# Optimization experiments

Hardware: AMD Instinct MI355X
Metric: run time of the kernel (lower is better)

Reference implementation:

```python
import jax, jax.numpy as jnp
import numpy as np

L, E, H, V = 12, 1024, 4096, 50277
LN_EPS = 9.999999747378752e-06  # tf float32 1e-5


def _layernorm(x, w, b):
    m = jnp.mean(x)
    xc = x - m
    return xc / jnp.sqrt(jnp.mean(xc * xc) + LN_EPS) * w + b


def setup_inputs() -> dict:
    key = jax.random.key(0)
    ks = jax.random.split(key, 32)
    f32 = jnp.float32

    def n(i, shape, s=0.02):
        return (jax.random.normal(ks[i], shape, f32) * s).astype(f32)

    inp = {
        "statea": n(0, (L, E), 0.3),
        "stateb": jax.random.uniform(ks[1], (L, E), f32),
        "statec": jax.random.uniform(ks[2], (L, E), f32),
        "stated": n(3, (L, E), 0.3),
        "preprocess": n(4, (V, E), 0.5),
        "ln1w": 1.0 + n(5, (L, E), 0.05),
        "ln1b": n(6, (L, E), 0.05),
        "ln2w": 1.0 + n(7, (L, E), 0.05),
        "ln2b": n(8, (L, E), 0.05),
        "att_key": n(9, (L, E, E)),
        "att_receptance": n(10, (L, E, E)),
        "att_value": n(11, (L, E, E)),
        "kktk": jax.random.uniform(ks[12], (L, E), f32),
        "vvtv": jax.random.uniform(ks[13], (L, E), f32),
        "rrtr": jax.random.uniform(ks[14], (L, E), f32),
        "time_first": n(15, (L, E), 0.2),
        "time_decay": n(16, (L, E), 0.2) - 1.0,
        "outputvv": n(17, (L, E, E)),
        "time_mix_k_ffn": jax.random.uniform(ks[18], (L, E), f32),
        "time_mix_r_ffn": jax.random.uniform(ks[19], (L, E), f32),
        "key_ffn": n(20, (L, H, E)),
        "receptance_ffn": n(21, (L, E, E)),
        "value_ffn": n(22, (L, E, H)),
        "post0": 1.0 + n(23, (E,), 0.05),
        "post1": n(24, (E,), 0.05),
        "post2": n(25, (V, E)),
        "token": 123,
    }
    return inp


def _forward(statea, stateb, statec, stated, preprocess, ln1w, ln1b, ln2w, ln2b,
             att_key, att_receptance, att_value, kktk, vvtv, rrtr, time_first,
             time_decay, outputvv, time_mix_k_ffn, time_mix_r_ffn, key_ffn,
             receptance_ffn, value_ffn, post0, post1, post2, token):
    x0 = preprocess[token]  # [E]

    def step(x, p):
        (sa, sb, sc, sd, l1w, l1b, l2w, l2b, ak, ar, av, kk, vv, rr,
         tfirst, tdecay, ovv, tmk_m, tmr_m, kf, rf, vf) = p
        xy = _layernorm(x, l1w, l1b)
        # WKV time-mixing (single step): mat-vecs + exp-decay state recursion
        k = jnp.exp(ak @ (xy + kk * sa))        # [E]
        v = av @ (xy + vv * sa)                 # [E]
        r = jnp.exp(ar @ (xy + rr * sa)) + 1.0  # [E]
        etf = jnp.exp(tfirst)
        w = sb + etf * k * v
        d = sc * r + etf * k * r
        mvv = ovv @ (w / (d + 0.001))           # [E]
        sxx = x + mvv
        aaa = xy
        etd = jnp.exp(tdecay)
        bbb = sb * etd + k * v
        ccc = sc * etd + k
        # channel-mixing FFN
        xx = _layernorm(sxx, l2w, l2b)
        kma = kf @ (xx + tmk_m * sd)            # [H]
        km = jnp.square(jnp.maximum(kma, 0.0))
        rt = jnp.exp(rf @ (xx + tmr_m * sd)) + 1.0  # [E]
        x_new = sxx + (vf @ km) / rt
        ddd = xx
        return x_new, (aaa, bbb, ccc, ddd)

    xs = (statea, stateb, statec, stated, ln1w, ln1b, ln2w, ln2b, att_key,
          att_receptance, att_value, kktk, vvtv, rrtr, time_first, time_decay,
          outputvv, time_mix_k_ffn, time_mix_r_ffn, key_ffn, receptance_ffn,
          value_ffn)
    xL, (aaa, bbb, ccc, ddd) = jax.lax.scan(step, x0, xs)
    logits = post2 @ _layernorm(xL, post0, post1)  # [V]
    return logits, aaa, bbb, ccc, ddd


def reference(statea, stateb, statec, stated, preprocess, ln1w, ln1b, ln2w, ln2b,
              att_key, att_receptance, att_value, kktk, vvtv, rrtr, time_first,
              time_decay, outputvv, time_mix_k_ffn, time_mix_r_ffn, key_ffn,
              receptance_ffn, value_ffn, post0, post1, post2, token):
    return _forward(statea, stateb, statec, stated, preprocess, ln1w, ln1b,
                    ln2w, ln2b, att_key, att_receptance, att_value, kktk, vvtv,
                    rrtr, time_first, time_decay, outputvv, time_mix_k_ffn,
                    time_mix_r_ffn, key_ffn, receptance_ffn, value_ffn, post0,
                    post1, post2, token)
```

## Files before the change

### kernel.cpp

```cpp
#include <hip/hip_runtime.h>
#include <math.h>


typedef unsigned long long u64;

constexpr int E = 1024;
constexpr int H = 4096;
constexpr int V = 50277;
constexpr int L = 12;
constexpr int NBLK = 256;
constexpr int NTHR = 512;
constexpr float LN_EPS = 9.999999747378752e-06f;

#define SCOPE_AGENT __HIP_MEMORY_SCOPE_AGENT

__device__ __forceinline__ u64 aload(const u64 *p) {
  return __hip_atomic_load(p, __ATOMIC_RELAXED, SCOPE_AGENT);
}
__device__ __forceinline__ void astore(u64 *p, u64 v) {
  __hip_atomic_store(p, v, __ATOMIC_RELAXED, SCOPE_AGENT);
}
__device__ __forceinline__ u64 mkw(unsigned ep, float f) {
  return ((u64)ep << 32) | (u64)__float_as_uint(f);
}
__device__ __forceinline__ float wpay(u64 v) { return __uint_as_float((unsigned)v); }
__device__ __forceinline__ bool freshw(u64 v, unsigned ep) {
  return (unsigned)(v >> 32) == ep;
}

__device__ __forceinline__ void lds_sync() {
  asm volatile("s_waitcnt lgkmcnt(0)" ::: "memory");
  __builtin_amdgcn_s_barrier();
}

struct Args {
  const float *statea, *stateb, *statec, *stated, *pre;
  const float *ln1w, *ln1b, *ln2w, *ln2b;
  const float *ak, *ar, *av, *kk, *vv, *rr, *tf, *td, *ovv;
  const float *tmk, *tmr, *kf, *rf, *vf;
  const float *post0, *post1, *post2;
  const int *token;
  float *out;
  u64 *wu, *wsx, *ssx, *wkm, *wx, *sxs;
};

__device__ __forceinline__ float wred(float v) {
#pragma unroll
  for (int off = 32; off; off >>= 1) v += __shfl_down(v, off, 64);
  return v;
}

__device__ __forceinline__ float dot4(float4 w, float4 x) {
  return w.x * x.x + w.y * x.y + w.z * x.z + w.w * x.w;
}

__device__ __forceinline__ float2 gather2(const u64 *wd, unsigned ep, int tid) {
  const u64 *p = wd + 2 * tid;
  u64 a0 = aload(p), a1 = aload(p + 1);
  while (!(freshw(a0, ep) & freshw(a1, ep))) {
    __builtin_amdgcn_s_sleep(1);
    a0 = aload(p); a1 = aload(p + 1);
  }
  return make_float2(wpay(a0), wpay(a1));
}

__device__ __forceinline__ void gather2s(const u64 *wd, const u64 *st, unsigned ep,
                                         int tid, float2 &v, float &sp) {
  const u64 *p = wd + 2 * tid;
  const u64 *q = st + tid;
  u64 a0 = aload(p), a1 = aload(p + 1), a2 = aload(q);
  while (!(freshw(a0, ep) & freshw(a1, ep) & freshw(a2, ep))) {
    __builtin_amdgcn_s_sleep(1);
    a0 = aload(p); a1 = aload(p + 1); a2 = aload(q);
  }
  v = make_float2(wpay(a0), wpay(a1));
  sp = wpay(a2);
}

__device__ __forceinline__ void gather8(const u64 *wd, unsigned ep, int tid,
                                        float4 &f0, float4 &f1) {
  const u64 *p = wd + 8 * tid;
  u64 b0, b1, b2, b3, b4, b5, b6, b7;
  for (;;) {
    b0 = aload(p);     b1 = aload(p + 1); b2 = aload(p + 2); b3 = aload(p + 3);
    b4 = aload(p + 4); b5 = aload(p + 5); b6 = aload(p + 6); b7 = aload(p + 7);
    bool ok = freshw(b0, ep) & freshw(b1, ep) & freshw(b2, ep) & freshw(b3, ep) &
              freshw(b4, ep) & freshw(b5, ep) & freshw(b6, ep) & freshw(b7, ep);
    if (ok) break;
    __builtin_amdgcn_s_sleep(1);
  }
  f0 = make_float4(wpay(b0), wpay(b1), wpay(b2), wpay(b3));
  f1 = make_float4(wpay(b4), wpay(b5), wpay(b6), wpay(b7));
}

__device__ __forceinline__ float2 stats_from_partials(float sp, float *s_red,
                                                      int lane, int wid) {
#pragma unroll
  for (int m = 2; m <= 32; m <<= 1) sp += __shfl_xor(sp, m, 64);
  if (lane < 2) s_red[wid * 2 + lane] = sp;
  lds_sync();
  float ts = 0.f, ts2 = 0.f;
#pragma unroll
  for (int i = 0; i < 8; ++i) { ts += s_red[2 * i]; ts2 += s_red[2 * i + 1]; }
  float m = ts * (1.0f / E);
  float var = ts2 * (1.0f / E) - m * m;
  return make_float2(m, rsqrtf(var + LN_EPS));
}

__device__ __forceinline__ float2 stats_full(float2 v, float *s_red, int lane, int wid) {
  float s = v.x + v.y, s2 = v.x * v.x + v.y * v.y;
#pragma unroll
  for (int m = 1; m <= 32; m <<= 1) {
    s += __shfl_xor(s, m, 64);
    s2 += __shfl_xor(s2, m, 64);
  }
  if (lane == 0) { s_red[wid * 2] = s; s_red[wid * 2 + 1] = s2; }
  lds_sync();
  float ts = 0.f, ts2 = 0.f;
#pragma unroll
  for (int i = 0; i < 8; ++i) { ts += s_red[2 * i]; ts2 += s_red[2 * i + 1]; }
  float m = ts * (1.0f / E);
  float var = ts2 * (1.0f / E) - m * m;
  return make_float2(m, rsqrtf(var + LN_EPS));
}

struct P1B {
  float4 w[6];
  float2 lw, lb, sa, kk, vv, rr;
  float tf, td, sb, sc;
};

__device__ __forceinline__ void load_p1(P1B &p, const Args &a, int l, int grow,
                                        int b0h, int tid, int blk) {
  const size_t lE = (size_t)l * E;
  const float4 *kr = reinterpret_cast<const float4 *>(a.ak + (lE + grow) * E);
  const float4 *vr = reinterpret_cast<const float4 *>(a.av + (lE + grow) * E);
  const float4 *rr4 = reinterpret_cast<const float4 *>(a.ar + (lE + grow) * E);
  p.w[0] = kr[b0h]; p.w[1] = kr[b0h + 64];
  p.w[2] = vr[b0h]; p.w[3] = vr[b0h + 64];
  p.w[4] = rr4[b0h]; p.w[5] = rr4[b0h + 64];
  p.lw = reinterpret_cast<const float2 *>(a.ln1w + lE)[tid];
  p.lb = reinterpret_cast<const float2 *>(a.ln1b + lE)[tid];
  p.sa = reinterpret_cast<const float2 *>(a.statea + lE)[tid];
  p.kk = reinterpret_cast<const float2 *>(a.kk + lE)[tid];
  p.vv = reinterpret_cast<const float2 *>(a.vv + lE)[tid];
  p.rr = reinterpret_cast<const float2 *>(a.rr + lE)[tid];
  if (tid < 4) {
    size_t o = lE + blk * 4 + tid;
    p.tf = a.tf[o]; p.td = a.td[o]; p.sb = a.stateb[o]; p.sc = a.statec[o];
  } else {
    p.tf = 0.f; p.td = 0.f; p.sb = 0.f; p.sc = 1.f;
  }
}

__device__ __forceinline__ void loadrow(float4 *d, const float4 *P, int r, int lane) {
  const float4 *p = P + (size_t)r * 256;
  d[0] = p[lane]; d[1] = p[lane + 64]; d[2] = p[lane + 128]; d[3] = p[lane + 192];
}

__global__ __launch_bounds__(NTHR, 2) void rwkv_fused(Args a) {
  __shared__ __align__(16) float s_a[4096];
  __shared__ __align__(16) float s_x[1024];
  __shared__ float s_red[16];
  __shared__ float s_pp[24];
  __shared__ float s_rt[4];

  const int tid = threadIdx.x;
  const int lane = tid & 63;
  const int wid = tid >> 6;
  const int blk = blockIdx.x;
  const int rloc = wid >> 1;
  const int h = wid & 1;
  const int grow = blk * 4 + rloc;
  const int b0h = h * 128 + lane;
  const int bv = h * 512 + lane;

  float *out_logits = a.out;
  float *out_aaa = a.out + V;
  float *out_bbb = out_aaa + L * E;
  float *out_ccc = out_bbb + L * E;
  float *out_ddd = out_ccc + L * E;

  const int tok = a.token[0];
  const float *pre_row = a.pre + (size_t)tok * E;
  const float4 *s4a = reinterpret_cast<const float4 *>(s_a);

  P1B p1;
  load_p1(p1, a, 0, grow, b0h, tid, blk);

#pragma unroll 1
  for (int l = 0; l < L; ++l) {
    const size_t lE = (size_t)l * E;
    const unsigned e1 = 4 * l + 1, e2 = 4 * l + 2, e3 = 4 * l + 3, e4 = 4 * l + 4;
    float4 pwo[2], pw3[10], pw4[8];
    float2 e3w, e3b, e3sd, e3tk, e3tr;

    {
      float2 xv; float2 st;
      if (l == 0) {
        xv = reinterpret_cast<const float2 *>(pre_row)[tid];
        reinterpret_cast<float2 *>(s_x)[tid] = xv;
        st = stats_full(xv, s_red, lane, wid);
      } else {
        float sp;
        gather2s(a.wx, a.sxs, 4 * l, tid, xv, sp);
        reinterpret_cast<float2 *>(s_x)[tid] = xv;
        st = stats_from_partials(sp, s_red, lane, wid);
      }
      float2 xy = make_float2((xv.x - st.x) * st.y * p1.lw.x + p1.lb.x,
                              (xv.y - st.x) * st.y * p1.lw.y + p1.lb.y);
      if ((tid >> 1) == blk) {
        out_aaa[lE + 2 * tid] = xy.x;
        out_aaa[lE + 2 * tid + 1] = xy.y;
      }
      reinterpret_cast<float2 *>(s_a)[tid] =
          make_float2(xy.x + p1.kk.x * p1.sa.x, xy.y + p1.kk.y * p1.sa.y);
      reinterpret_cast<float2 *>(s_a + 1024)[tid] =
          make_float2(xy.x + p1.vv.x * p1.sa.x, xy.y + p1.vv.y * p1.sa.y);
      reinterpret_cast<float2 *>(s_a + 2048)[tid] =
          make_float2(xy.x + p1.rr.x * p1.sa.x, xy.y + p1.rr.y * p1.sa.y);
      lds_sync();
      float accK = dot4(p1.w[0], s4a[b0h]) + dot4(p1.w[1], s4a[b0h + 64]);
      float accV = dot4(p1.w[2], s4a[256 + b0h]) + dot4(p1.w[3], s4a[256 + b0h + 64]);
      float accR = dot4(p1.w[4], s4a[512 + b0h]) + dot4(p1.w[5], s4a[512 + b0h + 64]);
      accK = wred(accK); accV = wred(accV); accR = wred(accR);
      if (lane == 0) {
        s_pp[wid * 3 + 0] = accK;
        s_pp[wid * 3 + 1] = accV;
        s_pp[wid * 3 + 2] = accR;
      }
      lds_sync();
      {
        const float4 *orow = reinterpret_cast<const float4 *>(a.ovv + (lE + grow) * E);
        pwo[0] = orow[b0h]; pwo[1] = orow[b0h + 64];
      }
      if (wid == 0) {
        int i = lane & 3;
        float K = s_pp[(2 * i) * 3] + s_pp[(2 * i + 1) * 3];
        float Vv = s_pp[(2 * i) * 3 + 1] + s_pp[(2 * i + 1) * 3 + 1];
        float R = s_pp[(2 * i) * 3 + 2] + s_pp[(2 * i + 1) * 3 + 2];
        float kx = expf(K), rx = expf(R) + 1.0f;
        float etf = expf(p1.tf), etd = expf(p1.td);
        float w_ = p1.sb + etf * kx * Vv;
        float d_ = p1.sc * rx + etf * kx * rx;
        float uv = w_ / (d_ + 0.001f);
        if (lane < 4) {
          size_t o = lE + blk * 4 + lane;
          astore(a.wu + blk * 4 + lane, mkw(e1, uv));
          out_bbb[o] = p1.sb * etd + kx * Vv;
          out_ccc[o] = p1.sc * etd + kx;
        }
      }
    }

    {
      float2 u2 = gather2(a.wu, e1, tid);
      reinterpret_cast<float2 *>(s_a)[tid] = u2;
      lds_sync();
      float acc = dot4(pwo[0], s4a[b0h]) + dot4(pwo[1], s4a[b0h + 64]);
      float x4 = s_x[blk * 4 + (lane & 3)];
      acc = wred(acc);
      if (lane == 0) s_pp[wid] = acc;
      lds_sync();
      {
        const float *kfb = a.kf + (size_t)l * H * E;
        const float4 *k0 = reinterpret_cast<const float4 *>(kfb + (size_t)(blk * 16 + wid) * E);
        const float4 *k1 = reinterpret_cast<const float4 *>(kfb + (size_t)(blk * 16 + 8 + wid) * E);
        pw3[0] = k0[lane];       pw3[1] = k0[lane + 64];
        pw3[2] = k0[lane + 128]; pw3[3] = k0[lane + 192];
        pw3[4] = k1[lane];       pw3[5] = k1[lane + 64];
        pw3[6] = k1[lane + 128]; pw3[7] = k1[lane + 192];
        const float4 *rrow = reinterpret_cast<const float4 *>(a.rf + (lE + grow) * E);
        pw3[8] = rrow[b0h]; pw3[9] = rrow[b0h + 64];
        e3w = reinterpret_cast<const float2 *>(a.ln2w + lE)[tid];
        e3b = reinterpret_cast<const float2 *>(a.ln2b + lE)[tid];
        e3sd = reinterpret_cast<const float2 *>(a.stated + lE)[tid];
        e3tk = reinterpret_cast<const float2 *>(a.tmk + lE)[tid];
        e3tr = reinterpret_cast<const float2 *>(a.tmr + lE)[tid];
      }
      if (wid == 0) {
        int i = lane & 3;
        float sxxv = x4 + s_pp[2 * i] + s_pp[2 * i + 1];
        float s0 = __shfl(sxxv, 0), s1 = __shfl(sxxv, 1);
        float s2v = __shfl(sxxv, 2), s3 = __shfl(sxxv, 3);
        float sum = s0 + s1 + s2v + s3;
        float ssq = s0 * s0 + s1 * s1 + s2v * s2v + s3 * s3;
        if (lane < 4) astore(a.wsx + blk * 4 + lane, mkw(e2, sxxv));
        if (lane == 0) astore(a.ssx + blk * 2 + 0, mkw(e2, sum));
        if (lane == 1) astore(a.ssx + blk * 2 + 1, mkw(e2, ssq));
      }
    }

    {
      float2 sxv; float sp;
      gather2s(a.wsx, a.ssx, e2, tid, sxv, sp);
      reinterpret_cast<float2 *>(s_x)[tid] = sxv;
      float2 st = stats_from_partials(sp, s_red, lane, wid);
      float2 xx = make_float2((sxv.x - st.x) * st.y * e3w.x + e3b.x,
                              (sxv.y - st.x) * st.y * e3w.y + e3b.y);
      if ((tid >> 1) == blk) {
        out_ddd[lE + 2 * tid] = xx.x;
        out_ddd[lE + 2 * tid + 1] = xx.y;
      }
      reinterpret_cast<float2 *>(s_a)[tid] =
          make_float2(xx.x + e3tk.x * e3sd.x, xx.y + e3tk.y * e3sd.y);
      reinterpret_cast<float2 *>(s_a + 1024)[tid] =
          make_float2(xx.x + e3tr.x * e3sd.x, xx.y + e3tr.y * e3sd.y);
      lds_sync();
      float k0 = 0.f, k1 = 0.f;
#pragma unroll
      for (int it = 0; it < 4; ++it) {
        float4 xv4 = s4a[it * 64 + lane];
        k0 += dot4(pw3[it], xv4);
        k1 += dot4(pw3[4 + it], xv4);
      }
      float ar_ = dot4(pw3[8], s4a[256 + b0h]) + dot4(pw3[9], s4a[256 + b0h + 64]);
      k0 = wred(k0); k1 = wred(k1); ar_ = wred(ar_);
      if (lane == 0) {
        float t0 = fmaxf(k0, 0.f), t1 = fmaxf(k1, 0.f);
        astore(a.wkm + blk * 16 + wid, mkw(e3, t0 * t0));
        astore(a.wkm + blk * 16 + 8 + wid, mkw(e3, t1 * t1));
        s_pp[wid] = ar_;
      }
      lds_sync();
      {
        const float4 *vrow = reinterpret_cast<const float4 *>(a.vf + (lE + grow) * H);
        pw4[0] = vrow[bv];       pw4[1] = vrow[bv + 64];
        pw4[2] = vrow[bv + 128]; pw4[3] = vrow[bv + 192];
        pw4[4] = vrow[bv + 256]; pw4[5] = vrow[bv + 320];
        pw4[6] = vrow[bv + 384]; pw4[7] = vrow[bv + 448];
      }
      if (tid < 4) s_rt[tid] = expf(s_pp[2 * tid] + s_pp[2 * tid + 1]) + 1.0f;
    }

    {
      float4 f0, f1;
      gather8(a.wkm, e3, tid, f0, f1);
      reinterpret_cast<float4 *>(s_a)[2 * tid] = f0;
      reinterpret_cast<float4 *>(s_a)[2 * tid + 1] = f1;
      lds_sync();
      float acc = 0.f;
#pragma unroll
      for (int it = 0; it < 8; ++it) acc += dot4(pw4[it], s4a[bv + it * 64]);
      float sx4 = s_x[blk * 4 + (lane & 3)];
      acc = wred(acc);
      if (lane == 0) s_pp[wid] = acc;
      lds_sync();
      if (l + 1 < L) {
        load_p1(p1, a, l + 1, grow, b0h, tid, blk);
      } else {
        p1.lw = reinterpret_cast<const float2 *>(a.post0)[tid];
        p1.lb = reinterpret_cast<const float2 *>(a.post1)[tid];
      }
      if (wid == 0) {
        int i = lane & 3;
        float xn = sx4 + (s_pp[2 * i] + s_pp[2 * i + 1]) / s_rt[i];
        float s0 = __shfl(xn, 0), s1 = __shfl(xn, 1);
        float s2v = __shfl(xn, 2), s3 = __shfl(xn, 3);
        float sum = s0 + s1 + s2v + s3;
        float ssq = s0 * s0 + s1 * s1 + s2v * s2v + s3 * s3;
        if (lane < 4) astore(a.wx + blk * 4 + lane, mkw(e4, xn));
        if (lane == 0) astore(a.sxs + blk * 2 + 0, mkw(e4, sum));
        if (lane == 1) astore(a.sxs + blk * 2 + 1, mkw(e4, ssq));
      }
    }
  }

  {
    float2 xv; float sp;
    gather2s(a.wx, a.sxs, 4 * L, tid, xv, sp);
    float2 st = stats_from_partials(sp, s_red, lane, wid);
    reinterpret_cast<float2 *>(s_a)[tid] =
        make_float2((xv.x - st.x) * st.y * p1.lw.x + p1.lb.x,
                    (xv.y - st.x) * st.y * p1.lw.y + p1.lb.y);
    lds_sync();

    const float4 *P2 = reinterpret_cast<const float4 *>(a.post2);
    const int gw = blk * 8 + wid;
    int r0 = gw, r1 = gw + 2048;
    float4 A0[4], A1[4];
    loadrow(A0, P2, r0, lane);
    loadrow(A1, P2, r1 < V ? r1 : r0, lane);
    while (true) {
      int n0 = r0 + 4096, n1 = n0 + 2048;
      bool more = n0 < V;
      float4 B0[4], B1[4];
      if (more) {
        loadrow(B0, P2, n0, lane);
        loadrow(B1, P2, n1 < V ? n1 : n0, lane);
      }
      float a0 = dot4(A0[0], s4a[lane]) + dot4(A0[1], s4a[lane + 64]) +
                 dot4(A0[2], s4a[lane + 128]) + dot4(A0[3], s4a[lane + 192]);
      float a1 = dot4(A1[0], s4a[lane]) + dot4(A1[1], s4a[lane + 64]) +
                 dot4(A1[2], s4a[lane + 128]) + dot4(A1[3], s4a[lane + 192]);
      a0 = wred(a0); a1 = wred(a1);
      if (lane == 0) {
        out_logits[r0] = a0;
        if (r1 < V) out_logits[r1] = a1;
      }
      if (!more) break;
#pragma unroll
      for (int q = 0; q < 4; ++q) { A0[q] = B0[q]; A1[q] = B1[q]; }
      r0 = n0; r1 = n1;
    }
  }
}

extern "C" void kernel_launch(void *const *d_in, const int *in_sizes, int n_in,
                              void *d_out, int out_size, void *d_ws, size_t ws_size,
                              hipStream_t stream) {
  (void)in_sizes; (void)n_in; (void)out_size; (void)ws_size;
  Args a;
  a.statea = (const float *)d_in[0];
  a.stateb = (const float *)d_in[1];
  a.statec = (const float *)d_in[2];
  a.stated = (const float *)d_in[3];
  a.pre    = (const float *)d_in[4];
  a.ln1w   = (const float *)d_in[5];
  a.ln1b   = (const float *)d_in[6];
  a.ln2w   = (const float *)d_in[7];
  a.ln2b   = (const float *)d_in[8];
  a.ak     = (const float *)d_in[9];
  a.ar     = (const float *)d_in[10];
  a.av     = (const float *)d_in[11];
  a.kk     = (const float *)d_in[12];
  a.vv     = (const float *)d_in[13];
  a.rr     = (const float *)d_in[14];
  a.tf     = (const float *)d_in[15];
  a.td     = (const float *)d_in[16];
  a.ovv    = (const float *)d_in[17];
  a.tmk    = (const float *)d_in[18];
  a.tmr    = (const float *)d_in[19];
  a.kf     = (const float *)d_in[20];
  a.rf     = (const float *)d_in[21];
  a.vf     = (const float *)d_in[22];
  a.post0  = (const float *)d_in[23];
  a.post1  = (const float *)d_in[24];
  a.post2  = (const float *)d_in[25];
  a.token  = (const int *)d_in[26];
  a.out    = (float *)d_out;

  u64 *wb = (u64 *)d_ws;
  a.wu  = wb;
  a.wsx = wb + 1024;
  a.ssx = wb + 2048;
  a.wkm = wb + 2560;
  a.wx  = wb + 6656;
  a.sxs = wb + 7680;
  hipMemsetAsync(d_ws, 0, 8192 * sizeof(u64), stream);
  rwkv_fused<<<NBLK, NTHR, 0, stream>>>(a);
}
```

Baseline: 302.3 us.

## Replace epoch-tagged data words with per-block flag barrier and plain payloads

Replaces the per-element epoch-tagged 64-bit words that consumers spin on with plain float payloads and one padded per-block epoch flag. Wave 0 drains its stores, publishes the flag and polls all 256 block flags, while the other waves prefetch the next stage's weights. Cross-block LayerNorm partial sums are dropped and every block recomputes full stats from the gathered vector. This cuts polled traffic and halves payload size, but turns fine-grained dataflow into a full grid barrier per stage and relies on relaxed-atomic ordering plus vmcnt drains for correctness.

```diff
diff --git a/kernel.cpp b/kernel.cpp
--- a/kernel.cpp
+++ b/kernel.cpp
@@ -3,6 +3,7 @@
 
 
 typedef unsigned long long u64;
+typedef unsigned u32;
 
 constexpr int E = 1024;
 constexpr int H = 4096;
@@ -12,25 +13,29 @@
 constexpr int NTHR = 512;
 constexpr float LN_EPS = 9.999999747378752e-06f;
 
-#define SCOPE_AGENT __HIP_MEMORY_SCOPE_AGENT
-
-__device__ __forceinline__ u64 aload(const u64 *p) {
-  return __hip_atomic_load(p, __ATOMIC_RELAXED, SCOPE_AGENT);
-}
-__device__ __forceinline__ void astore(u64 *p, u64 v) {
-  __hip_atomic_store(p, v, __ATOMIC_RELAXED, SCOPE_AGENT);
-}
-__device__ __forceinline__ u64 mkw(unsigned ep, float f) {
-  return ((u64)ep << 32) | (u64)__float_as_uint(f);
-}
-__device__ __forceinline__ float wpay(u64 v) { return __uint_as_float((unsigned)v); }
-__device__ __forceinline__ bool freshw(u64 v, unsigned ep) {
-  return (unsigned)(v >> 32) == ep;
+#define SA __HIP_MEMORY_SCOPE_AGENT
+
+__device__ __forceinline__ void stf(float *p, float v) {
+  __hip_atomic_store(p, v, __ATOMIC_RELAXED, SA);
+}
+__device__ __forceinline__ void stu(u32 *p, u32 v) {
+  __hip_atomic_store(p, v, __ATOMIC_RELAXED, SA);
+}
+__device__ __forceinline__ u32 ldu(const u32 *p) {
+  return __hip_atomic_load(p, __ATOMIC_RELAXED, SA);
+}
+__device__ __forceinline__ float2 ld2(const float *p) {
+  union { u64 u; float2 f; } c;
+  c.u = __hip_atomic_load((const u64 *)p, __ATOMIC_RELAXED, SA);
+  return c.f;
 }
 
 __device__ __forceinline__ void lds_sync() {
   asm volatile("s_waitcnt lgkmcnt(0)" ::: "memory");
   __builtin_amdgcn_s_barrier();
+}
+__device__ __forceinline__ void vdrain() {
+  asm volatile("s_waitcnt vmcnt(0)" ::: "memory");
 }
 
 struct Args {
@@ -41,7 +46,8 @@
   const float *post0, *post1, *post2;
   const int *token;
   float *out;
-  u64 *wu, *wsx, *ssx, *wkm, *wx, *sxs;
+  u32 *flags;
+  float *wu, *wsx, *wx, *wkm;
 };
 
 __device__ __forceinline__ float wred(float v) {
@@ -49,79 +55,8 @@
   for (int off = 32; off; off >>= 1) v += __shfl_down(v, off, 64);
   return v;
 }
-
 __device__ __forceinline__ float dot4(float4 w, float4 x) {
   return w.x * x.x + w.y * x.y + w.z * x.z + w.w * x.w;
-}
-
-__device__ __forceinline__ float2 gather2(const u64 *wd, unsigned ep, int tid) {
-  const u64 *p = wd + 2 * tid;
-  u64 a0 = aload(p), a1 = aload(p + 1);
-  while (!(freshw(a0, ep) & freshw(a1, ep))) {
-    __builtin_amdgcn_s_sleep(1);
-    a0 = aload(p); a1 = aload(p + 1);
-  }
-  return make_float2(wpay(a0), wpay(a1));
-}
-
-__device__ __forceinline__ void gather2s(const u64 *wd, const u64 *st, unsigned ep,
-                                         int tid, float2 &v, float &sp) {
-  const u64 *p = wd + 2 * tid;
-  const u64 *q = st + tid;
-  u64 a0 = aload(p), a1 = aload(p + 1), a2 = aload(q);
-  while (!(freshw(a0, ep) & freshw(a1, ep) & freshw(a2, ep))) {
-    __builtin_amdgcn_s_sleep(1);
-    a0 = aload(p); a1 = aload(p + 1); a2 = aload(q);
-  }
-  v = make_float2(wpay(a0), wpay(a1));
-  sp = wpay(a2);
-}
-
-__device__ __forceinline__ void gather8(const u64 *wd, unsigned ep, int tid,
-                                        float4 &f0, float4 &f1) {
-  const u64 *p = wd + 8 * tid;
-  u64 b0, b1, b2, b3, b4, b5, b6, b7;
-  for (;;) {
-    b0 = aload(p);     b1 = aload(p + 1); b2 = aload(p + 2); b3 = aload(p + 3);
-    b4 = aload(p + 4); b5 = aload(p + 5); b6 = aload(p + 6); b7 = aload(p + 7);
-    bool ok = freshw(b0, ep) & freshw(b1, ep) & freshw(b2, ep) & freshw(b3, ep) &
-              freshw(b4, ep) & freshw(b5, ep) & freshw(b6, ep) & freshw(b7, ep);
-    if (ok) break;
-    __builtin_amdgcn_s_sleep(1);
-  }
-  f0 = make_float4(wpay(b0), wpay(b1), wpay(b2), wpay(b3));
-  f1 = make_float4(wpay(b4), wpay(b5), wpay(b6), wpay(b7));
-}
-
-__device__ __forceinline__ float2 stats_from_partials(float sp, float *s_red,
-                                                      int lane, int wid) {
-#pragma unroll
-  for (int m = 2; m <= 32; m <<= 1) sp += __shfl_xor(sp, m, 64);
-  if (lane < 2) s_red[wid * 2 + lane] = sp;
-  lds_sync();
-  float ts = 0.f, ts2 = 0.f;
-#pragma unroll
-  for (int i = 0; i < 8; ++i) { ts += s_red[2 * i]; ts2 += s_red[2 * i + 1]; }
-  float m = ts * (1.0f / E);
-  float var = ts2 * (1.0f / E) - m * m;
-  return make_float2(m, rsqrtf(var + LN_EPS));
-}
-
-__device__ __forceinline__ float2 stats_full(float2 v, float *s_red, int lane, int wid) {
-  float s = v.x + v.y, s2 = v.x * v.x + v.y * v.y;
-#pragma unroll
-  for (int m = 1; m <= 32; m <<= 1) {
-    s += __shfl_xor(s, m, 64);
-    s2 += __shfl_xor(s2, m, 64);
-  }
-  if (lane == 0) { s_red[wid * 2] = s; s_red[wid * 2 + 1] = s2; }
-  lds_sync();
-  float ts = 0.f, ts2 = 0.f;
-#pragma unroll
-  for (int i = 0; i < 8; ++i) { ts += s_red[2 * i]; ts2 += s_red[2 * i + 1]; }
-  float m = ts * (1.0f / E);
-  float var = ts2 * (1.0f / E) - m * m;
-  return make_float2(m, rsqrtf(var + LN_EPS));
 }
 
 struct P1B {
@@ -129,7 +64,6 @@
   float2 lw, lb, sa, kk, vv, rr;
   float tf, td, sb, sc;
 };
-
 __device__ __forceinline__ void load_p1(P1B &p, const Args &a, int l, int grow,
                                         int b0h, int tid, int blk) {
   const size_t lE = (size_t)l * E;
@@ -152,6 +86,55 @@
     p.tf = 0.f; p.td = 0.f; p.sb = 0.f; p.sc = 1.f;
   }
 }
+__device__ __forceinline__ void load_ovv_kf0(float4 po[2], float4 pf[8],
+                                             const Args &a, int l, int grow,
+                                             int b0h, int blk, int wid, int lane) {
+  const size_t lE = (size_t)l * E;
+  const float4 *orow = reinterpret_cast<const float4 *>(a.ovv + (lE + grow) * E);
+  po[0] = orow[b0h]; po[1] = orow[b0h + 64];
+  const float *kfb = a.kf + (size_t)l * H * E;
+  const float4 *k0 = reinterpret_cast<const float4 *>(kfb + (size_t)(blk * 16 + wid) * E);
+  pf[0] = k0[lane]; pf[1] = k0[lane + 64]; pf[2] = k0[lane + 128]; pf[3] = k0[lane + 192];
+}
+struct P3B {
+  float4 r[2];
+  float2 lw, lb, sd, tk, tr;
+};
+__device__ __forceinline__ void load_kf1_rf(float4 pf[8], P3B &p, const Args &a,
+                                            int l, int grow, int b0h, int blk,
+                                            int wid, int lane, int tid) {
+  const size_t lE = (size_t)l * E;
+  const float *kfb = a.kf + (size_t)l * H * E;
+  const float4 *k1 = reinterpret_cast<const float4 *>(kfb + (size_t)(blk * 16 + 8 + wid) * E);
+  pf[4] = k1[lane]; pf[5] = k1[lane + 64]; pf[6] = k1[lane + 128]; pf[7] = k1[lane + 192];
+  const float4 *rrow = reinterpret_cast<const float4 *>(a.rf + (lE + grow) * E);
+  p.r[0] = rrow[b0h]; p.r[1] = rrow[b0h + 64];
+  p.lw = reinterpret_cast<const float2 *>(a.ln2w + lE)[tid];
+  p.lb = reinterpret_cast<const float2 *>(a.ln2b + lE)[tid];
+  p.sd = reinterpret_cast<const float2 *>(a.stated + lE)[tid];
+  p.tk = reinterpret_cast<const float2 *>(a.tmk + lE)[tid];
+  p.tr = reinterpret_cast<const float2 *>(a.tmr + lE)[tid];
+}
+__device__ __forceinline__ void load_vf(float4 pv[8], const Args &a, int l,
+                                        int grow, int bv) {
+  const float4 *vrow = reinterpret_cast<const float4 *>(a.vf + ((size_t)l * E + grow) * H);
+  pv[0] = vrow[bv];       pv[1] = vrow[bv + 64];
+  pv[2] = vrow[bv + 128]; pv[3] = vrow[bv + 192];
+  pv[4] = vrow[bv + 256]; pv[5] = vrow[bv + 320];
+  pv[6] = vrow[bv + 384]; pv[7] = vrow[bv + 448];
+}
+
+__device__ __forceinline__ void poll_flags(const u32 *flags, unsigned ep, int lane) {
+  const u32 *f0 = flags + (lane * 4 + 0) * 32;
+  const u32 *f1 = flags + (lane * 4 + 1) * 32;
+  const u32 *f2 = flags + (lane * 4 + 2) * 32;
+  const u32 *f3 = flags + (lane * 4 + 3) * 32;
+  for (;;) {
+    u32 a0 = ldu(f0), a1 = ldu(f1), a2 = ldu(f2), a3 = ldu(f3);
+    if (a0 >= ep && a1 >= ep && a2 >= ep && a3 >= ep) break;
+    __builtin_amdgcn_s_sleep(1);
+  }
+}
 
 __device__ __forceinline__ void loadrow(float4 *d, const float4 *P, int r, int lane) {
   const float4 *p = P + (size_t)r * 256;
@@ -186,29 +169,37 @@
   const float4 *s4a = reinterpret_cast<const float4 *>(s_a);
 
   P1B p1;
+  float4 po[2], pf[8], pv[8];
+  P3B p3;
+  unsigned ep = 1;
+
   load_p1(p1, a, 0, grow, b0h, tid, blk);
 
 #pragma unroll 1
   for (int l = 0; l < L; ++l) {
     const size_t lE = (size_t)l * E;
-    const unsigned e1 = 4 * l + 1, e2 = 4 * l + 2, e3 = 4 * l + 3, e4 = 4 * l + 4;
-    float4 pwo[2], pw3[10], pw4[8];
-    float2 e3w, e3b, e3sd, e3tk, e3tr;
 
     {
-      float2 xv; float2 st;
-      if (l == 0) {
-        xv = reinterpret_cast<const float2 *>(pre_row)[tid];
-        reinterpret_cast<float2 *>(s_x)[tid] = xv;
-        st = stats_full(xv, s_red, lane, wid);
-      } else {
-        float sp;
-        gather2s(a.wx, a.sxs, 4 * l, tid, xv, sp);
-        reinterpret_cast<float2 *>(s_x)[tid] = xv;
-        st = stats_from_partials(sp, s_red, lane, wid);
-      }
-      float2 xy = make_float2((xv.x - st.x) * st.y * p1.lw.x + p1.lb.x,
-                              (xv.y - st.x) * st.y * p1.lw.y + p1.lb.y);
+      float2 xv;
+      if (l == 0) xv = reinterpret_cast<const float2 *>(pre_row)[tid];
+      else        xv = ld2(a.wx + 2 * tid);
+      if (wid != 0) load_ovv_kf0(po, pf, a, l, grow, b0h, blk, wid, lane);
+      reinterpret_cast<float2 *>(s_x)[tid] = xv;
+      float s = xv.x + xv.y, s2 = xv.x * xv.x + xv.y * xv.y;
+#pragma unroll
+      for (int m = 1; m <= 32; m <<= 1) {
+        s += __shfl_xor(s, m, 64);
+        s2 += __shfl_xor(s2, m, 64);
+      }
+      if (lane == 0) { s_red[wid * 2] = s; s_red[wid * 2 + 1] = s2; }
+      lds_sync();
+      float ts = 0.f, ts2 = 0.f;
+#pragma unroll
+      for (int i = 0; i < 8; ++i) { ts += s_red[2 * i]; ts2 += s_red[2 * i + 1]; }
+      float mn = ts * (1.0f / E);
+      float rstd = rsqrtf(ts2 * (1.0f / E) - mn * mn + LN_EPS);
+      float2 xy = make_float2((xv.x - mn) * rstd * p1.lw.x + p1.lb.x,
+                              (xv.y - mn) * rstd * p1.lw.y + p1.lb.y);
       if ((tid >> 1) == blk) {
         out_aaa[lE + 2 * tid] = xy.x;
         out_aaa[lE + 2 * tid + 1] = xy.y;
@@ -230,149 +221,175 @@
         s_pp[wid * 3 + 2] = accR;
       }
       lds_sync();
-      {
-        const float4 *orow = reinterpret_cast<const float4 *>(a.ovv + (lE + grow) * E);
-        pwo[0] = orow[b0h]; pwo[1] = orow[b0h + 64];
-      }
       if (wid == 0) {
         int i = lane & 3;
         float K = s_pp[(2 * i) * 3] + s_pp[(2 * i + 1) * 3];
         float Vv = s_pp[(2 * i) * 3 + 1] + s_pp[(2 * i + 1) * 3 + 1];
         float R = s_pp[(2 * i) * 3 + 2] + s_pp[(2 * i + 1) * 3 + 2];
-        float kx = expf(K), rx = expf(R) + 1.0f;
-        float etf = expf(p1.tf), etd = expf(p1.td);
-        float w_ = p1.sb + etf * kx * Vv;
-        float d_ = p1.sc * rx + etf * kx * rx;
-        float uv = w_ / (d_ + 0.001f);
         if (lane < 4) {
           size_t o = lE + blk * 4 + lane;
-          astore(a.wu + blk * 4 + lane, mkw(e1, uv));
+          float kx = expf(K), rx = expf(R) + 1.0f;
+          float etf = expf(p1.tf), etd = expf(p1.td);
+          float w_ = p1.sb + etf * kx * Vv;
+          float d_ = p1.sc * rx + etf * kx * rx;
+          stf(a.wu + blk * 4 + lane, w_ / (d_ + 0.001f));
           out_bbb[o] = p1.sb * etd + kx * Vv;
           out_ccc[o] = p1.sc * etd + kx;
         }
-      }
+        vdrain();
+        if (lane == 0) stu(a.flags + blk * 32, ep);
+        load_ovv_kf0(po, pf, a, l, grow, b0h, blk, wid, lane);
+        poll_flags(a.flags, ep, lane);
+      }
+      lds_sync(); ++ep;
     }
 
     {
-      float2 u2 = gather2(a.wu, e1, tid);
+      float2 u2 = ld2(a.wu + 2 * tid);
+      if (wid != 0) load_kf1_rf(pf, p3, a, l, grow, b0h, blk, wid, lane, tid);
       reinterpret_cast<float2 *>(s_a)[tid] = u2;
       lds_sync();
-      float acc = dot4(pwo[0], s4a[b0h]) + dot4(pwo[1], s4a[b0h + 64]);
-      float x4 = s_x[blk * 4 + (lane & 3)];
+      float acc = dot4(po[0], s4a[b0h]) + dot4(po[1], s4a[b0h + 64]);
       acc = wred(acc);
       if (lane == 0) s_pp[wid] = acc;
       lds_sync();
-      {
-        const float *kfb = a.kf + (size_t)l * H * E;
-        const float4 *k0 = reinterpret_cast<const float4 *>(kfb + (size_t)(blk * 16 + wid) * E);
-        const float4 *k1 = reinterpret_cast<const float4 *>(kfb + (size_t)(blk * 16 + 8 + wid) * E);
-        pw3[0] = k0[lane];       pw3[1] = k0[lane + 64];
-        pw3[2] = k0[lane + 128]; pw3[3] = k0[lane + 192];
-        pw3[4] = k1[lane];       pw3[5] = k1[lane + 64];
-        pw3[6] = k1[lane + 128]; pw3[7] = k1[lane + 192];
-        const float4 *rrow = reinterpret_cast<const float4 *>(a.rf + (lE + grow) * E);
-        pw3[8] = rrow[b0h]; pw3[9] = rrow[b0h + 64];
-        e3w = reinterpret_cast<const float2 *>(a.ln2w + lE)[tid];
-        e3b = reinterpret_cast<const float2 *>(a.ln2b + lE)[tid];
-        e3sd = reinterpret_cast<const float2 *>(a.stated + lE)[tid];
-        e3tk = reinterpret_cast<const float2 *>(a.tmk + lE)[tid];
-        e3tr = reinterpret_cast<const float2 *>(a.tmr + lE)[tid];
-      }
       if (wid == 0) {
         int i = lane & 3;
-        float sxxv = x4 + s_pp[2 * i] + s_pp[2 * i + 1];
-        float s0 = __shfl(sxxv, 0), s1 = __shfl(sxxv, 1);
-        float s2v = __shfl(sxxv, 2), s3 = __shfl(sxxv, 3);
-        float sum = s0 + s1 + s2v + s3;
-        float ssq = s0 * s0 + s1 * s1 + s2v * s2v + s3 * s3;
-        if (lane < 4) astore(a.wsx + blk * 4 + lane, mkw(e2, sxxv));
-        if (lane == 0) astore(a.ssx + blk * 2 + 0, mkw(e2, sum));
-        if (lane == 1) astore(a.ssx + blk * 2 + 1, mkw(e2, ssq));
-      }
+        float sxx = s_x[blk * 4 + i] + s_pp[2 * i] + s_pp[2 * i + 1];
+        if (lane < 4) stf(a.wsx + blk * 4 + lane, sxx);
+        vdrain();
+        if (lane == 0) stu(a.flags + blk * 32, ep);
+        load_kf1_rf(pf, p3, a, l, grow, b0h, blk, wid, lane, tid);
+        poll_flags(a.flags, ep, lane);
+      }
+      lds_sync(); ++ep;
     }
 
     {
-      float2 sxv; float sp;
-      gather2s(a.wsx, a.ssx, e2, tid, sxv, sp);
+      float2 sxv = ld2(a.wsx + 2 * tid);
+      if (wid != 0) load_vf(pv, a, l, grow, bv);
       reinterpret_cast<float2 *>(s_x)[tid] = sxv;
-      float2 st = stats_from_partials(sp, s_red, lane, wid);
-      float2 xx = make_float2((sxv.x - st.x) * st.y * e3w.x + e3b.x,
-                              (sxv.y - st.x) * st.y * e3w.y + e3b.y);
+      float s = sxv.x + sxv.y, s2 = sxv.x * sxv.x + sxv.y * sxv.y;
+#pragma unroll
+      for (int m = 1; m <= 32; m <<= 1) {
+        s += __shfl_xor(s, m, 64);
+        s2 += __shfl_xor(s2, m, 64);
+      }
+      if (lane == 0) { s_red[wid * 2] = s; s_red[wid * 2 + 1] = s2; }
+      lds_sync();
+      float ts = 0.f, ts2 = 0.f;
+#pragma unroll
+      for (int i = 0; i < 8; ++i) { ts += s_red[2 * i]; ts2 += s_red[2 * i + 1]; }
+      float mn = ts * (1.0f / E);
+      float rstd = rsqrtf(ts2 * (1.0f / E) - mn * mn + LN_EPS);
+      float2 xx = make_float2((sxv.x - mn) * rstd * p3.lw.x + p3.lb.x,
+                              (sxv.y - mn) * rstd * p3.lw.y + p3.lb.y);
       if ((tid >> 1) == blk) {
         out_ddd[lE + 2 * tid] = xx.x;
         out_ddd[lE + 2 * tid + 1] = xx.y;
       }
       reinterpret_cast<float2 *>(s_a)[tid] =
-          make_float2(xx.x + e3tk.x * e3sd.x, xx.y + e3tk.y * e3sd.y);
+          make_float2(xx.x + p3.tk.x * p3.sd.x, xx.y + p3.tk.y * p3.sd.y);
       reinterpret_cast<float2 *>(s_a + 1024)[tid] =
-          make_float2(xx.x + e3tr.x * e3sd.x, xx.y + e3tr.y * e3sd.y);
+          make_float2(xx.x + p3.tr.x * p3.sd.x, xx.y + p3.tr.y * p3.sd.y);
       lds_sync();
       float k0 = 0.f, k1 = 0.f;
 #pragma unroll
       for (int it = 0; it < 4; ++it) {
         float4 xv4 = s4a[it * 64 + lane];
-        k0 += dot4(pw3[it], xv4);
-        k1 += dot4(pw3[4 + it], xv4);
-      }
-      float ar_ = dot4(pw3[8], s4a[256 + b0h]) + dot4(pw3[9], s4a[256 + b0h + 64]);
+        k0 += dot4(pf[it], xv4);
+        k1 += dot4(pf[4 + it], xv4);
+      }
+      float ar_ = dot4(p3.r[0], s4a[256 + b0h]) + dot4(p3.r[1], s4a[256 + b0h + 64]);
       k0 = wred(k0); k1 = wred(k1); ar_ = wred(ar_);
       if (lane == 0) {
-        float t0 = fmaxf(k0, 0.f), t1 = fmaxf(k1, 0.f);
-        astore(a.wkm + blk * 16 + wid, mkw(e3, t0 * t0));
-        astore(a.wkm + blk * 16 + 8 + wid, mkw(e3, t1 * t1));
-        s_pp[wid] = ar_;
-      }
-      lds_sync();
-      {
-        const float4 *vrow = reinterpret_cast<const float4 *>(a.vf + (lE + grow) * H);
-        pw4[0] = vrow[bv];       pw4[1] = vrow[bv + 64];
-        pw4[2] = vrow[bv + 128]; pw4[3] = vrow[bv + 192];
-        pw4[4] = vrow[bv + 256]; pw4[5] = vrow[bv + 320];
-        pw4[6] = vrow[bv + 384]; pw4[7] = vrow[bv + 448];
-      }
-      if (tid < 4) s_rt[tid] = expf(s_pp[2 * tid] + s_pp[2 * tid + 1]) + 1.0f;
+        s_pp[wid * 3 + 0] = k0;
+        s_pp[wid * 3 + 1] = k1;
+        s_pp[wid * 3 + 2] = ar_;
+      }
+      lds_sync();
+      if (wid == 0) {
+        if (lane < 4) {
+          float arsum = s_pp[(2 * lane) * 3 + 2] + s_pp[(2 * lane + 1) * 3 + 2];
+          s_rt[lane] = expf(arsum) + 1.0f;
+        }
+        if (lane < 16) {
+          int w = lane & 7, sel = (lane >> 3) & 1;
+          float kv = s_pp[w * 3 + sel];
+          float t = fmaxf(kv, 0.f);
+          stf(a.wkm + blk * 16 + sel * 8 + w, t * t);
+        }
+        vdrain();
+        if (lane == 0) stu(a.flags + blk * 32, ep);
+        load_vf(pv, a, l, grow, bv);
+        poll_flags(a.flags, ep, lane);
+      }
+      lds_sync(); ++ep;
     }
 
     {
-      float4 f0, f1;
-      gather8(a.wkm, e3, tid, f0, f1);
-      reinterpret_cast<float4 *>(s_a)[2 * tid] = f0;
-      reinterpret_cast<float4 *>(s_a)[2 * tid + 1] = f1;
+      const u64 *km64 = reinterpret_cast<const u64 *>(a.wkm);
+      union { u64 u; float2 f; } g0, g1, g2, g3;
+      g0.u = __hip_atomic_load(km64 + 2 * tid, __ATOMIC_RELAXED, SA);
+      g1.u = __hip_atomic_load(km64 + 2 * tid + 1, __ATOMIC_RELAXED, SA);
+      g2.u = __hip_atomic_load(km64 + 1024 + 2 * tid, __ATOMIC_RELAXED, SA);
+      g3.u = __hip_atomic_load(km64 + 1024 + 2 * tid + 1, __ATOMIC_RELAXED, SA);
+      if (wid != 0) {
+        if (l + 1 < L) {
+          load_p1(p1, a, l + 1, grow, b0h, tid, blk);
+        } else {
+          p1.lw = reinterpret_cast<const float2 *>(a.post0)[tid];
+          p1.lb = reinterpret_cast<const float2 *>(a.post1)[tid];
+        }
+      }
+      reinterpret_cast<float2 *>(s_a)[2 * tid] = g0.f;
+      reinterpret_cast<float2 *>(s_a)[2 * tid + 1] = g1.f;
+      reinterpret_cast<float2 *>(s_a)[1024 + 2 * tid] = g2.f;
+      reinterpret_cast<float2 *>(s_a)[1024 + 2 * tid + 1] = g3.f;
       lds_sync();
       float acc = 0.f;
 #pragma unroll
-      for (int it = 0; it < 8; ++it) acc += dot4(pw4[it], s4a[bv + it * 64]);
-      float sx4 = s_x[blk * 4 + (lane & 3)];
+      for (int it = 0; it < 8; ++it) acc += dot4(pv[it], s4a[bv + it * 64]);
       acc = wred(acc);
       if (lane == 0) s_pp[wid] = acc;
       lds_sync();
-      if (l + 1 < L) {
-        load_p1(p1, a, l + 1, grow, b0h, tid, blk);
-      } else {
-        p1.lw = reinterpret_cast<const float2 *>(a.post0)[tid];
-        p1.lb = reinterpret_cast<const float2 *>(a.post1)[tid];
-      }
       if (wid == 0) {
         int i = lane & 3;
-        float xn = sx4 + (s_pp[2 * i] + s_pp[2 * i + 1]) / s_rt[i];
-        float s0 = __shfl(xn, 0), s1 = __shfl(xn, 1);
-        float s2v = __shfl(xn, 2), s3 = __shfl(xn, 3);
-        float sum = s0 + s1 + s2v + s3;
-        float ssq = s0 * s0 + s1 * s1 + s2v * s2v + s3 * s3;
-        if (lane < 4) astore(a.wx + blk * 4 + lane, mkw(e4, xn));
-        if (lane == 0) astore(a.sxs + blk * 2 + 0, mkw(e4, sum));
-        if (lane == 1) astore(a.sxs + blk * 2 + 1, mkw(e4, ssq));
-      }
+        float xn = s_x[blk * 4 + i] + (s_pp[2 * i] + s_pp[2 * i + 1]) / s_rt[i];
+        if (lane < 4) stf(a.wx + blk * 4 + lane, xn);
+        vdrain();
+        if (lane == 0) stu(a.flags + blk * 32, ep);
+        if (l + 1 < L) {
+          load_p1(p1, a, l + 1, grow, b0h, tid, blk);
+        } else {
+          p1.lw = reinterpret_cast<const float2 *>(a.post0)[tid];
+          p1.lb = reinterpret_cast<const float2 *>(a.post1)[tid];
+        }
+        poll_flags(a.flags, ep, lane);
+      }
+      lds_sync(); ++ep;
     }
   }
 
   {
-    float2 xv; float sp;
-    gather2s(a.wx, a.sxs, 4 * L, tid, xv, sp);
-    float2 st = stats_from_partials(sp, s_red, lane, wid);
+    float2 xv = ld2(a.wx + 2 * tid);
+    reinterpret_cast<float2 *>(s_x)[tid] = xv;
+    float s = xv.x + xv.y, s2 = xv.x * xv.x + xv.y * xv.y;
+#pragma unroll
+    for (int m = 1; m <= 32; m <<= 1) {
+      s += __shfl_xor(s, m, 64);
+      s2 += __shfl_xor(s2, m, 64);
+    }
+    if (lane == 0) { s_red[wid * 2] = s; s_red[wid * 2 + 1] = s2; }
+    lds_sync();
+    float ts = 0.f, ts2 = 0.f;
+#pragma unroll
+    for (int i = 0; i < 8; ++i) { ts += s_red[2 * i]; ts2 += s_red[2 * i + 1]; }
+    float mn = ts * (1.0f / E);
+    float rstd = rsqrtf(ts2 * (1.0f / E) - mn * mn + LN_EPS);
     reinterpret_cast<float2 *>(s_a)[tid] =
-        make_float2((xv.x - st.x) * st.y * p1.lw.x + p1.lb.x,
-                    (xv.y - st.x) * st.y * p1.lw.y + p1.lb.y);
+        make_float2((xv.x - mn) * rstd * p1.lw.x + p1.lb.x,
+                    (xv.y - mn) * rstd * p1.lw.y + p1.lb.y);
     lds_sync();
 
     const float4 *P2 = reinterpret_cast<const float4 *>(a.post2);
@@ -440,13 +457,13 @@
   a.token  = (const int *)d_in[26];
   a.out    = (float *)d_out;
 
-  u64 *wb = (u64 *)d_ws;
-  a.wu  = wb;
-  a.wsx = wb + 1024;
-  a.ssx = wb + 2048;
-  a.wkm = wb + 2560;
-  a.wx  = wb + 6656;
-  a.sxs = wb + 7680;
-  hipMemsetAsync(d_ws, 0, 8192 * sizeof(u64), stream);
+  a.flags = (u32 *)d_ws;
+  float *base = (float *)((char *)d_ws + 32768);
+  a.wu  = base;
+  a.wsx = base + 1024;
+  a.wx  = base + 2048;
+  a.wkm = base + 3072;
+
+  hipMemsetAsync(d_ws, 0, 32768, stream);
   rwkv_fused<<<NBLK, NTHR, 0, stream>>>(a);
 }
```

Result: slower. 330.7 us (+9.4%).
